# Optimization experiments

Hardware: AMD Instinct MI355X
Metric: run time of the kernel (lower is better)

## Reference

```python
import jax, jax.numpy as jnp
import numpy as np

FFT_SIZE = 16384

def setup_inputs() -> dict:
    key = jax.random.key(0)
    k1, k2 = jax.random.split(key)
    u = jax.random.normal(k1, (8, 1024, 8192), dtype=jnp.float32)
    k = jax.random.normal(k2, (1024, 8192), dtype=jnp.float32)
    return {"u": u, "k": k}

def reference(u, k):
    # Faithful port of PyTorchFFTConv.forward with fft_size=FFT_SIZE.
    L = u.shape[-1]
    u_f32 = u.astype(jnp.float32)
    k_f32 = k.astype(jnp.float32)
    if k_f32.ndim == 2:
        k_f32 = k_f32[None]  # (1, H, L) -> broadcasts over batch
    u_fft = jnp.fft.rfft(u_f32, n=FFT_SIZE, axis=-1)   # (B, H, fft/2+1) complex64
    k_fft = jnp.fft.rfft(k_f32, n=FFT_SIZE, axis=-1)
    y_fft = u_fft * k_fft / FFT_SIZE
    # irfft with norm='forward' (no 1/n on inverse) combined with the /fft_s above
    # yields the standard circular convolution, matching the torch code exactly.
    y = jnp.fft.irfft(y_fft, n=FFT_SIZE, axis=-1, norm='forward')
    return y[..., :L].astype(jnp.float32)
```

## Files before the change

### kernel.cpp

```cpp
#include <hip/hip_runtime.h>

#define NFFT 16384
#define LSIG 8192
#define NH   1024
#define NTH  512
#define LDSC (NFFT + ((NFFT >> 5) << 1))

__device__ __forceinline__ int PADC(int i) { return i + ((i >> 5) << 1); }
__device__ __forceinline__ int PADI(int i) { return i + (i >> 5); }

struct cplx { float x, y; };
__device__ __forceinline__ cplx cadd(cplx a, cplx b){ return {a.x+b.x, a.y+b.y}; }
__device__ __forceinline__ cplx csub(cplx a, cplx b){ return {a.x-b.x, a.y-b.y}; }
__device__ __forceinline__ cplx cmul(cplx a, cplx b){ return {a.x*b.x - a.y*b.y, a.x*b.y + a.y*b.x}; }

template<int V> struct ic { static constexpr int value = V; };
template<int Start, int End, typename F>
__device__ __forceinline__ void cfor(F&& f) {
  if constexpr (Start < End) { f(ic<Start>{}); cfor<Start+1, End>(static_cast<F&&>(f)); }
}

constexpr float W32C32[32] = {
  1.0f, 0.9807852804f, 0.9238795325f, 0.8314696123f,
  0.7071067812f, 0.5555702330f, 0.3826834324f, 0.1950903220f,
  0.0f, -0.1950903220f, -0.3826834324f, -0.5555702330f,
  -0.7071067812f, -0.8314696123f, -0.9238795325f, -0.9807852804f,
  -1.0f, -0.9807852804f, -0.9238795325f, -0.8314696123f,
  -0.7071067812f, -0.5555702330f, -0.3826834324f, -0.1950903220f,
  0.0f, 0.1950903220f, 0.3826834324f, 0.5555702330f,
  0.7071067812f, 0.8314696123f, 0.9238795325f, 0.9807852804f };
constexpr float W32S32[32] = {
  0.0f, 0.1950903220f, 0.3826834324f, 0.5555702330f,
  0.7071067812f, 0.8314696123f, 0.9238795325f, 0.9807852804f,
  1.0f, 0.9807852804f, 0.9238795325f, 0.8314696123f,
  0.7071067812f, 0.5555702330f, 0.3826834324f, 0.1950903220f,
  0.0f, -0.1950903220f, -0.3826834324f, -0.5555702330f,
  -0.7071067812f, -0.8314696123f, -0.9238795325f, -0.9807852804f,
  -1.0f, -0.9807852804f, -0.9238795325f, -0.8314696123f,
  -0.7071067812f, -0.5555702330f, -0.3826834324f, -0.1950903220f };
constexpr int BR3[8] = {0,4,2,6,1,5,3,7};

template<int KK, bool INV>
__device__ __forceinline__ cplx twid(cplx d) {
  constexpr int K = KK & 31;
  if constexpr (K == 0)       return d;
  else if constexpr (K == 8)  { if constexpr (INV) return cplx{-d.y, d.x}; else return cplx{d.y, -d.x}; }
  else if constexpr (K == 16) return cplx{-d.x, -d.y};
  else if constexpr (K == 24) { if constexpr (INV) return cplx{d.y, -d.x}; else return cplx{-d.y, d.x}; }
  else {
    constexpr float c = W32C32[K];
    constexpr float s = INV ? W32S32[K] : -W32S32[K];
    return cmul(d, cplx{c, s});
  }
}

template<int N, int SP, bool INV>
__device__ __forceinline__ void fft_pass(cplx* z) {
  #pragma unroll
  for (int b = 0; b < N; b += 2*SP) {
    cfor<0, SP>([&](auto rc){
      constexpr int r = decltype(rc)::value;
      constexpr int KK = r * (16 / SP);
      if constexpr (!INV) {
        cplx u = z[b+r], v = z[b+r+SP];
        z[b+r]    = cadd(u, v);
        z[b+r+SP] = twid<KK,false>(csub(u, v));
      } else {
        cplx t0 = z[b+r], t1 = z[b+r+SP];
        cplx w = twid<KK,true>(t1);
        z[b+r]    = cadd(t0, w);
        z[b+r+SP] = csub(t0, w);
      }
    });
  }
}

template<int N, bool INV>
__device__ __forceinline__ void fft_regs(cplx* z) {
  if constexpr (!INV) {
    if constexpr (N >= 32) fft_pass<N,16,false>(z);
    if constexpr (N >= 16) fft_pass<N, 8,false>(z);
    if constexpr (N >=  8) fft_pass<N, 4,false>(z);
    if constexpr (N >=  4) fft_pass<N, 2,false>(z);
    fft_pass<N,1,false>(z);
  } else {
    fft_pass<N,1,true>(z);
    if constexpr (N >=  4) fft_pass<N, 2,true>(z);
    if constexpr (N >=  8) fft_pass<N, 4,true>(z);
    if constexpr (N >= 16) fft_pass<N, 8,true>(z);
    if constexpr (N >= 32) fft_pass<N,16,true>(z);
  }
}

template<int S, bool INV>
__device__ __forceinline__ void stage8p(float2* sz, int tid) {
  const float ang1 = (INV ? 2.0f : -2.0f) * 3.14159265358979f / (float)(8 * S);
  #pragma unroll 1
  for (int it = 0; it < 2; ++it) {
    int pp = tid + it * NTH;
    int bf = 2 * pp;
    int q = bf / S;
    int r = bf - q * S;
    int base = q * (8 * S) + r;
    float ta = ang1 * (float)r;
    float tb = ang1 * (float)(r + 1);
    cplx w1a = {__cosf(ta), __sinf(ta)};
    cplx w1b = {__cosf(tb), __sinf(tb)};
    cplx wa[8], wb[8];
    wa[1]=w1a; wa[2]=cmul(w1a,w1a); wa[3]=cmul(wa[2],w1a); wa[4]=cmul(wa[2],wa[2]);
    wa[5]=cmul(wa[4],wa[1]); wa[6]=cmul(wa[4],wa[2]); wa[7]=cmul(wa[4],wa[3]);
    wb[1]=w1b; wb[2]=cmul(w1b,w1b); wb[3]=cmul(wb[2],w1b); wb[4]=cmul(wb[2],wb[2]);
    wb[5]=cmul(wb[4],wb[1]); wb[6]=cmul(wb[4],wb[2]); wb[7]=cmul(wb[4],wb[3]);

    cplx A[8], B[8];
    if constexpr (!INV) {
      cfor<0,8>([&](auto jc){ constexpr int j = decltype(jc)::value;
        float4 v = *reinterpret_cast<const float4*>(&sz[PADC(base + j*S)]);
        A[j] = {v.x, v.y}; B[j] = {v.z, v.w}; });
      fft_regs<8,false>(A);
      fft_regs<8,false>(B);
      cfor<0,8>([&](auto pc){ constexpr int p = decltype(pc)::value;
        constexpr int m = BR3[p];
        cplx oa, ob;
        if constexpr (m == 0) { oa = A[p]; ob = B[p]; }
        else { oa = cmul(A[p], wa[m]); ob = cmul(B[p], wb[m]); }
        *reinterpret_cast<float4*>(&sz[PADC(base + m*S)]) = make_float4(oa.x, oa.y, ob.x, ob.y); });
    } else {
      cfor<0,8>([&](auto pc){ constexpr int p = decltype(pc)::value;
        constexpr int m = BR3[p];
        float4 v = *reinterpret_cast<const float4*>(&sz[PADC(base + m*S)]);
        if constexpr (m == 0) { A[p] = {v.x, v.y}; B[p] = {v.z, v.w}; }
        else { A[p] = cmul(cplx{v.x, v.y}, wa[m]); B[p] = cmul(cplx{v.z, v.w}, wb[m]); } });
      fft_regs<8,true>(A);
      fft_regs<8,true>(B);
      cfor<0,8>([&](auto jc){ constexpr int j = decltype(jc)::value;
        *reinterpret_cast<float4*>(&sz[PADC(base + j*S)]) = make_float4(A[j].x, A[j].y, B[j].x, B[j].y); });
    }
  }
}

template<bool INV>
__device__ __forceinline__ void stage8_s4p(float2* sz, int tid) {
  cfor<0,2>([&](auto rrc){
    constexpr int r0 = decltype(rrc)::value * 2;
    int base = tid * 32 + r0;
    cplx A[8], B[8];
    if constexpr (!INV) {
      cfor<0,8>([&](auto jc){ constexpr int j = decltype(jc)::value;
        float4 v = *reinterpret_cast<const float4*>(&sz[PADC(base + j*4)]);
        A[j] = {v.x, v.y}; B[j] = {v.z, v.w}; });
      fft_regs<8,false>(A);
      fft_regs<8,false>(B);
      cfor<0,8>([&](auto pc){ constexpr int p = decltype(pc)::value;
        constexpr int m = BR3[p];
        cplx oa = twid<r0*m, false>(A[p]);
        cplx ob = twid<(r0+1)*m, false>(B[p]);
        *reinterpret_cast<float4*>(&sz[PADC(base + m*4)]) = make_float4(oa.x, oa.y, ob.x, ob.y); });
    } else {
      cfor<0,8>([&](auto pc){ constexpr int p = decltype(pc)::value;
        constexpr int m = BR3[p];
        float4 v = *reinterpret_cast<const float4*>(&sz[PADC(base + m*4)]);
        A[p] = twid<r0*m, true>(cplx{v.x, v.y});
        B[p] = twid<(r0+1)*m, true>(cplx{v.z, v.w}); });
      fft_regs<8,true>(A);
      fft_regs<8,true>(B);
      cfor<0,8>([&](auto jc){ constexpr int j = decltype(jc)::value;
        *reinterpret_cast<float4*>(&sz[PADC(base + j*4)]) = make_float4(A[j].x, A[j].y, B[j].x, B[j].y); });
    }
  });
}

__global__ __launch_bounds__(NTH)
void kfft_kernel(const float* __restrict__ kin, float2* __restrict__ kh) {
  __shared__ __align__(16) float2 sz[LDSC];
  const int tid = threadIdx.x;
  const int h = blockIdx.x;
  const float* krow = kin + (size_t)h * LSIG;
  #pragma unroll
  for (int c = 0; c < 8; ++c) {
    int ci = (c * NTH + tid) * 2;
    float2 v = *reinterpret_cast<const float2*>(krow + ci);
    *reinterpret_cast<float4*>(&sz[PADC(ci)]) = make_float4(v.x, 0.f, v.y, 0.f);
    *reinterpret_cast<float4*>(&sz[PADC(ci + LSIG)]) = make_float4(0.f, 0.f, 0.f, 0.f);
  }
  __syncthreads();
  stage8p<2048,false>(sz, tid); __syncthreads();
  stage8p< 256,false>(sz, tid); __syncthreads();
  stage8p<  32,false>(sz, tid); __syncthreads();
  stage8_s4p<false>(sz, tid);   __syncthreads();

  const float scl = 1.0f / (float)NFFT;
  float2* row = kh + (size_t)h * NFFT;
  #pragma unroll
  for (int s = 0; s < 8; ++s) {
    int m = tid + NTH * s;
    int ci = 4 * m;
    float4 f0 = *reinterpret_cast<const float4*>(&sz[PADC(ci)]);
    float4 f1 = *reinterpret_cast<const float4*>(&sz[PADC(ci + 2)]);
    cplx z[4] = { {f0.x, f0.y}, {f0.z, f0.w}, {f1.x, f1.y}, {f1.z, f1.w} };
    fft_regs<4,false>(z);
    *reinterpret_cast<float4*>(row + ci)     = make_float4(z[0].x*scl, z[0].y*scl, z[1].x*scl, z[1].y*scl);
    *reinterpret_cast<float4*>(row + ci + 2) = make_float4(z[2].x*scl, z[2].y*scl, z[3].x*scl, z[3].y*scl);
  }
}

__global__ __launch_bounds__(NTH)
void conv_kernel(const float* __restrict__ u, const float2* __restrict__ kh,
                 float* __restrict__ out) {
  __shared__ __align__(16) float2 sz[LDSC];
  const int tid = threadIdx.x;
  const int bid = blockIdx.x;
  const int h  = bid >> 2;
  const int pr = bid & 3;

  const float* u0 = u + ((size_t)(2*pr) * NH + h) * LSIG;
  const float* u1 = u0 + (size_t)NH * LSIG;
  #pragma unroll
  for (int c = 0; c < 8; ++c) {
    int ci = (c * NTH + tid) * 2;
    float2 a = *reinterpret_cast<const float2*>(u0 + ci);
    float2 b = *reinterpret_cast<const float2*>(u1 + ci);
    *reinterpret_cast<float4*>(&sz[PADC(ci)]) = make_float4(a.x, b.x, a.y, b.y);
    *reinterpret_cast<float4*>(&sz[PADC(ci + LSIG)]) = make_float4(0.f, 0.f, 0.f, 0.f);
  }
  __syncthreads();
  stage8p<2048,false>(sz, tid); __syncthreads();
  stage8p< 256,false>(sz, tid); __syncthreads();
  stage8p<  32,false>(sz, tid); __syncthreads();
  stage8_s4p<false>(sz, tid);   __syncthreads();

  {
    const float2* krow = kh + (size_t)h * NFFT;
    #pragma unroll
    for (int s = 0; s < 8; ++s) {
      int m = tid + NTH * s;
      int ci = 4 * m;
      float4 f0 = *reinterpret_cast<const float4*>(&sz[PADC(ci)]);
      float4 f1 = *reinterpret_cast<const float4*>(&sz[PADC(ci + 2)]);
      cplx z[4] = { {f0.x, f0.y}, {f0.z, f0.w}, {f1.x, f1.y}, {f1.z, f1.w} };
      fft_regs<4,false>(z);
      float4 k0 = *reinterpret_cast<const float4*>(krow + ci);
      float4 k1 = *reinterpret_cast<const float4*>(krow + ci + 2);
      z[0] = cmul(z[0], cplx{k0.x, k0.y});
      z[1] = cmul(z[1], cplx{k0.z, k0.w});
      z[2] = cmul(z[2], cplx{k1.x, k1.y});
      z[3] = cmul(z[3], cplx{k1.z, k1.w});
      fft_regs<4,true>(z);
      *reinterpret_cast<float4*>(&sz[PADC(ci)])     = make_float4(z[0].x, z[0].y, z[1].x, z[1].y);
      *reinterpret_cast<float4*>(&sz[PADC(ci + 2)]) = make_float4(z[2].x, z[2].y, z[3].x, z[3].y);
    }
  }
  __syncthreads();
  stage8_s4p<true>(sz, tid);   __syncthreads();
  stage8p<  32,true>(sz, tid); __syncthreads();
  stage8p< 256,true>(sz, tid); __syncthreads();
  stage8p<2048,true>(sz, tid); __syncthreads();

  float* o0 = out + ((size_t)(2*pr) * NH + h) * LSIG;
  float* o1 = o0 + (size_t)NH * LSIG;
  #pragma unroll
  for (int c = 0; c < 4; ++c) {
    int ci = (c * NTH + tid) * 4;
    float4 f0 = *reinterpret_cast<const float4*>(&sz[PADC(ci)]);
    float4 f1 = *reinterpret_cast<const float4*>(&sz[PADC(ci + 2)]);
    *reinterpret_cast<float4*>(o0 + ci) = make_float4(f0.x, f0.z, f1.x, f1.z);
    *reinterpret_cast<float4*>(o1 + ci) = make_float4(f0.y, f0.w, f1.y, f1.w);
  }
}

template<int S, bool INV>
__device__ __forceinline__ void stage8f(float* sre, float* sim, int tid) {
  const float ang1 = (INV ? 2.0f : -2.0f) * 3.14159265358979f / (float)(8 * S);
  #pragma unroll
  for (int it = 0; it < (NFFT/8)/NTH; ++it) {
    int bf = tid + it * NTH;
    int q = bf / S;
    int r = bf - q * S;
    int base = q * (8 * S) + r;
    float t = ang1 * (float)r;
    cplx w1 = {__cosf(t), __sinf(t)};
    cplx wp[8];
    wp[0] = {1.0f, 0.0f};
    wp[1] = w1; wp[2] = cmul(w1, w1); wp[3] = cmul(wp[2], w1); wp[4] = cmul(wp[2], wp[2]);
    wp[5] = cmul(wp[4], wp[1]); wp[6] = cmul(wp[4], wp[2]); wp[7] = cmul(wp[4], wp[3]);
    cplx a[8];
    if constexpr (!INV) {
      cfor<0,8>([&](auto jc){ constexpr int j = decltype(jc)::value;
        int idx = PADI(base + j*S); a[j] = {sre[idx], sim[idx]}; });
      fft_regs<8,false>(a);
      cfor<0,8>([&](auto pc){ constexpr int p = decltype(pc)::value;
        constexpr int m = BR3[p];
        cplx o; if constexpr (m == 0) o = a[p]; else o = cmul(a[p], wp[m]);
        int idx = PADI(base + m*S); sre[idx] = o.x; sim[idx] = o.y; });
    } else {
      cfor<0,8>([&](auto pc){ constexpr int p = decltype(pc)::value;
        constexpr int m = BR3[p];
        int idx = PADI(base + m*S); cplx v = {sre[idx], sim[idx]};
        if constexpr (m == 0) a[p] = v; else a[p] = cmul(v, wp[m]); });
      fft_regs<8,true>(a);
      cfor<0,8>([&](auto jc){ constexpr int j = decltype(jc)::value;
        int idx = PADI(base + j*S); sre[idx] = a[j].x; sim[idx] = a[j].y; });
    }
  }
}

template<bool INV>
__device__ __forceinline__ void stage8_s4f(float* sre, float* sim, int tid) {
  cfor<0,4>([&](auto rc){
    constexpr int r = decltype(rc)::value;
    int base = tid * 32 + r;
    cplx a[8];
    if constexpr (!INV) {
      cfor<0,8>([&](auto jc){ constexpr int j = decltype(jc)::value;
        int idx = PADI(base + j*4); a[j] = {sre[idx], sim[idx]}; });
      fft_regs<8,false>(a);
      cfor<0,8>([&](auto pc){ constexpr int p = decltype(pc)::value;
        constexpr int m = BR3[p];
        cplx o = twid<r*m, false>(a[p]);
        int idx = PADI(base + m*4); sre[idx] = o.x; sim[idx] = o.y; });
    } else {
      cfor<0,8>([&](auto pc){ constexpr int p = decltype(pc)::value;
        constexpr int m = BR3[p];
        int idx = PADI(base + m*4); cplx v = {sre[idx], sim[idx]};
        a[p] = twid<r*m, true>(v); });
      fft_regs<8,true>(a);
      cfor<0,8>([&](auto jc){ constexpr int j = decltype(jc)::value;
        int idx = PADI(base + j*4); sre[idx] = a[j].x; sim[idx] = a[j].y; });
    }
  });
}

__global__ __launch_bounds__(NTH)
void fftconv_fallback(const float* __restrict__ u, const float* __restrict__ kin,
                      float* __restrict__ out) {
  __shared__ float sre[NFFT + (NFFT >> 5)];
  __shared__ float sim[NFFT + (NFFT >> 5)];
  const int tid = threadIdx.x;
  const int bid = blockIdx.x;
  const int h  = bid >> 2;
  const int pr = bid & 3;

  const float* krow = kin + (size_t)h * LSIG;
  #pragma unroll
  for (int c = 0; c < 4; ++c) {
    int i0 = (c * NTH + tid) * 4;
    float4 v = *reinterpret_cast<const float4*>(krow + i0);
    int p0 = PADI(i0);
    sre[p0+0]=v.x; sre[p0+1]=v.y; sre[p0+2]=v.z; sre[p0+3]=v.w;
    sim[p0+0]=0.f; sim[p0+1]=0.f; sim[p0+2]=0.f; sim[p0+3]=0.f;
    int p1 = PADI(i0 + LSIG);
    sre[p1+0]=0.f; sre[p1+1]=0.f; sre[p1+2]=0.f; sre[p1+3]=0.f;
    sim[p1+0]=0.f; sim[p1+1]=0.f; sim[p1+2]=0.f; sim[p1+3]=0.f;
  }
  __syncthreads();
  stage8f<2048,false>(sre, sim, tid); __syncthreads();
  stage8f< 256,false>(sre, sim, tid); __syncthreads();
  stage8f<  32,false>(sre, sim, tid); __syncthreads();
  stage8_s4f<false>(sre, sim, tid);   __syncthreads();

  cplx kq[4][4];
  cplx kq2[4][4];
  const float scl = 1.0f / (float)NFFT;
  #pragma unroll
  for (int s = 0; s < 8; ++s) {
    int m = tid + NTH * s;
    int p = PADI(4 * m);
    cplx z[4] = { {sre[p+0], sim[p+0]}, {sre[p+1], sim[p+1]},
                  {sre[p+2], sim[p+2]}, {sre[p+3], sim[p+3]} };
    fft_regs<4,false>(z);
    #pragma unroll
    for (int e = 0; e < 4; ++e) {
      cplx v = {z[e].x*scl, z[e].y*scl};
      if (s < 4) kq[s][e] = v; else kq2[s-4][e] = v;
    }
  }
  __syncthreads();

  const float* u0 = u + ((size_t)(2*pr) * NH + h) * LSIG;
  const float* u1 = u0 + (size_t)NH * LSIG;
  #pragma unroll
  for (int c = 0; c < 4; ++c) {
    int i0 = (c * NTH + tid) * 4;
    float4 a = *reinterpret_cast<const float4*>(u0 + i0);
    float4 b = *reinterpret_cast<const float4*>(u1 + i0);
    int p0 = PADI(i0);
    sre[p0+0]=a.x; sre[p0+1]=a.y; sre[p0+2]=a.z; sre[p0+3]=a.w;
    sim[p0+0]=b.x; sim[p0+1]=b.y; sim[p0+2]=b.z; sim[p0+3]=b.w;
    int p1 = PADI(i0 + LSIG);
    sre[p1+0]=0.f; sre[p1+1]=0.f; sre[p1+2]=0.f; sre[p1+3]=0.f;
    sim[p1+0]=0.f; sim[p1+1]=0.f; sim[p1+2]=0.f; sim[p1+3]=0.f;
  }
  __syncthreads();
  stage8f<2048,false>(sre, sim, tid); __syncthreads();
  stage8f< 256,false>(sre, sim, tid); __syncthreads();
  stage8f<  32,false>(sre, sim, tid); __syncthreads();
  stage8_s4f<false>(sre, sim, tid);   __syncthreads();

  #pragma unroll
  for (int s = 0; s < 8; ++s) {
    int m = tid + NTH * s;
    int p = PADI(4 * m);
    cplx z[4] = { {sre[p+0], sim[p+0]}, {sre[p+1], sim[p+1]},
                  {sre[p+2], sim[p+2]}, {sre[p+3], sim[p+3]} };
    fft_regs<4,false>(z);
    #pragma unroll
    for (int e = 0; e < 4; ++e) z[e] = cmul(z[e], (s<4) ? kq[s][e] : kq2[s-4][e]);
    fft_regs<4,true>(z);
    #pragma unroll
    for (int e = 0; e < 4; ++e) { sre[p+e] = z[e].x; sim[p+e] = z[e].y; }
  }
  __syncthreads();
  stage8_s4f<true>(sre, sim, tid);   __syncthreads();
  stage8f<  32,true>(sre, sim, tid); __syncthreads();
  stage8f< 256,true>(sre, sim, tid); __syncthreads();
  stage8f<2048,true>(sre, sim, tid); __syncthreads();

  float* o0 = out + ((size_t)(2*pr) * NH + h) * LSIG;
  float* o1 = o0 + (size_t)NH * LSIG;
  #pragma unroll
  for (int c = 0; c < 4; ++c) {
    int i0 = (c * NTH + tid) * 4;
    int p0 = PADI(i0);
    float4 a = {sre[p0], sre[p0+1], sre[p0+2], sre[p0+3]};
    float4 b = {sim[p0], sim[p0+1], sim[p0+2], sim[p0+3]};
    *reinterpret_cast<float4*>(o0 + i0) = a;
    *reinterpret_cast<float4*>(o1 + i0) = b;
  }
}

extern "C" void kernel_launch(void* const* d_in, const int* in_sizes, int n_in,
                              void* d_out, int out_size, void* d_ws, size_t ws_size,
                              hipStream_t stream) {
  (void)in_sizes; (void)n_in; (void)out_size;
  const float* u = (const float*)d_in[0];
  const float* k = (const float*)d_in[1];
  float* out = (float*)d_out;
  const size_t need = (size_t)NH * NFFT * sizeof(float2);
  if (ws_size >= need) {
    hipLaunchKernelGGL(kfft_kernel, dim3(NH),   dim3(NTH), 0, stream, k, (float2*)d_ws);
    hipLaunchKernelGGL(conv_kernel, dim3(4096), dim3(NTH), 0, stream, u, (const float2*)d_ws, out);
  } else {
    hipLaunchKernelGGL(fftconv_fallback, dim3(4096), dim3(NTH), 0, stream, u, k, out);
  }
}
```

Baseline: 444.6 us.

## Fuse first FFT stage with global load and last inverse stage with store

The first radix-8 stage is now computed in registers straight from global memory. It exploits the zero-padded upper half, so only 4 inputs per butterfly are loaded and the LDS zero-fill is skipped. The final inverse stage is fused with the output write and computes only the needed first half of outputs. The last-stage data mapping is also changed so each thread owns contiguous chunks, which drops two barriers around the pointwise multiply. The cost is extra register pressure and a less coalesced global access pattern (strided float2 loads per thread).

```diff
diff --git a/kernel.cpp b/kernel.cpp
--- a/kernel.cpp
+++ b/kernel.cpp
@@ -176,25 +176,45 @@
   const int tid = threadIdx.x;
   const int h = blockIdx.x;
   const float* krow = kin + (size_t)h * LSIG;
-  #pragma unroll
-  for (int c = 0; c < 8; ++c) {
-    int ci = (c * NTH + tid) * 2;
-    float2 v = *reinterpret_cast<const float2*>(krow + ci);
-    *reinterpret_cast<float4*>(&sz[PADC(ci)]) = make_float4(v.x, 0.f, v.y, 0.f);
-    *reinterpret_cast<float4*>(&sz[PADC(ci + LSIG)]) = make_float4(0.f, 0.f, 0.f, 0.f);
-  }
-  __syncthreads();
-  stage8p<2048,false>(sz, tid); __syncthreads();
+  const float ang1 = -2.0f * 3.14159265358979f / (float)NFFT;
+
+  #pragma unroll 1
+  for (int it = 0; it < 2; ++it) {
+    int base = 2*tid + 1024*it;
+    cplx A[8], B[8];
+    cfor<0,4>([&](auto jc){ constexpr int j = decltype(jc)::value;
+      float2 kr = *reinterpret_cast<const float2*>(krow + base + j*2048);
+      A[j] = {kr.x, 0.f}; B[j] = {kr.y, 0.f}; });
+    cfor<0,4>([&](auto jc){ constexpr int j = decltype(jc)::value;
+      A[j+4] = twid<4*j,false>(A[j]);
+      B[j+4] = twid<4*j,false>(B[j]); });
+    fft_pass<8,2,false>(A); fft_pass<8,1,false>(A);
+    fft_pass<8,2,false>(B); fft_pass<8,1,false>(B);
+    float ta = ang1 * (float)base, tb = ang1 * (float)(base + 1);
+    cplx w1a = {__cosf(ta), __sinf(ta)};
+    cplx w1b = {__cosf(tb), __sinf(tb)};
+    cplx wa[8], wb[8];
+    wa[1]=w1a; wa[2]=cmul(w1a,w1a); wa[3]=cmul(wa[2],w1a); wa[4]=cmul(wa[2],wa[2]);
+    wa[5]=cmul(wa[4],wa[1]); wa[6]=cmul(wa[4],wa[2]); wa[7]=cmul(wa[4],wa[3]);
+    wb[1]=w1b; wb[2]=cmul(w1b,w1b); wb[3]=cmul(wb[2],w1b); wb[4]=cmul(wb[2],wb[2]);
+    wb[5]=cmul(wb[4],wb[1]); wb[6]=cmul(wb[4],wb[2]); wb[7]=cmul(wb[4],wb[3]);
+    cfor<0,8>([&](auto pc){ constexpr int p = decltype(pc)::value;
+      constexpr int m = BR3[p];
+      cplx oa, ob;
+      if constexpr (m == 0) { oa = A[p]; ob = B[p]; }
+      else { oa = cmul(A[p], wa[m]); ob = cmul(B[p], wb[m]); }
+      *reinterpret_cast<float4*>(&sz[PADC(base + m*2048)]) = make_float4(oa.x, oa.y, ob.x, ob.y); });
+  }
+  __syncthreads();
   stage8p< 256,false>(sz, tid); __syncthreads();
   stage8p<  32,false>(sz, tid); __syncthreads();
-  stage8_s4p<false>(sz, tid);   __syncthreads();
+  stage8_s4p<false>(sz, tid);
 
   const float scl = 1.0f / (float)NFFT;
   float2* row = kh + (size_t)h * NFFT;
   #pragma unroll
   for (int s = 0; s < 8; ++s) {
-    int m = tid + NTH * s;
-    int ci = 4 * m;
+    int ci = 32*tid + 4*s;
     float4 f0 = *reinterpret_cast<const float4*>(&sz[PADC(ci)]);
     float4 f1 = *reinterpret_cast<const float4*>(&sz[PADC(ci + 2)]);
     cplx z[4] = { {f0.x, f0.y}, {f0.z, f0.w}, {f1.x, f1.y}, {f1.z, f1.w} };
@@ -215,26 +235,50 @@
 
   const float* u0 = u + ((size_t)(2*pr) * NH + h) * LSIG;
   const float* u1 = u0 + (size_t)NH * LSIG;
-  #pragma unroll
-  for (int c = 0; c < 8; ++c) {
-    int ci = (c * NTH + tid) * 2;
-    float2 a = *reinterpret_cast<const float2*>(u0 + ci);
-    float2 b = *reinterpret_cast<const float2*>(u1 + ci);
-    *reinterpret_cast<float4*>(&sz[PADC(ci)]) = make_float4(a.x, b.x, a.y, b.y);
-    *reinterpret_cast<float4*>(&sz[PADC(ci + LSIG)]) = make_float4(0.f, 0.f, 0.f, 0.f);
-  }
-  __syncthreads();
-  stage8p<2048,false>(sz, tid); __syncthreads();
+  float* o0 = out + ((size_t)(2*pr) * NH + h) * LSIG;
+  float* o1 = o0 + (size_t)NH * LSIG;
+
+  {
+    const float ang1 = -2.0f * 3.14159265358979f / (float)NFFT;
+    #pragma unroll 1
+    for (int it = 0; it < 2; ++it) {
+      int base = 2*tid + 1024*it;
+      cplx A[8], B[8];
+      cfor<0,4>([&](auto jc){ constexpr int j = decltype(jc)::value;
+        float2 a2 = *reinterpret_cast<const float2*>(u0 + base + j*2048);
+        float2 b2 = *reinterpret_cast<const float2*>(u1 + base + j*2048);
+        A[j] = {a2.x, b2.x}; B[j] = {a2.y, b2.y}; });
+      cfor<0,4>([&](auto jc){ constexpr int j = decltype(jc)::value;
+        A[j+4] = twid<4*j,false>(A[j]);
+        B[j+4] = twid<4*j,false>(B[j]); });
+      fft_pass<8,2,false>(A); fft_pass<8,1,false>(A);
+      fft_pass<8,2,false>(B); fft_pass<8,1,false>(B);
+      float ta = ang1 * (float)base, tb = ang1 * (float)(base + 1);
+      cplx w1a = {__cosf(ta), __sinf(ta)};
+      cplx w1b = {__cosf(tb), __sinf(tb)};
+      cplx wa[8], wb[8];
+      wa[1]=w1a; wa[2]=cmul(w1a,w1a); wa[3]=cmul(wa[2],w1a); wa[4]=cmul(wa[2],wa[2]);
+      wa[5]=cmul(wa[4],wa[1]); wa[6]=cmul(wa[4],wa[2]); wa[7]=cmul(wa[4],wa[3]);
+      wb[1]=w1b; wb[2]=cmul(w1b,w1b); wb[3]=cmul(wb[2],w1b); wb[4]=cmul(wb[2],wb[2]);
+      wb[5]=cmul(wb[4],wb[1]); wb[6]=cmul(wb[4],wb[2]); wb[7]=cmul(wb[4],wb[3]);
+      cfor<0,8>([&](auto pc){ constexpr int p = decltype(pc)::value;
+        constexpr int m = BR3[p];
+        cplx oa, ob;
+        if constexpr (m == 0) { oa = A[p]; ob = B[p]; }
+        else { oa = cmul(A[p], wa[m]); ob = cmul(B[p], wb[m]); }
+        *reinterpret_cast<float4*>(&sz[PADC(base + m*2048)]) = make_float4(oa.x, oa.y, ob.x, ob.y); });
+    }
+  }
+  __syncthreads();
   stage8p< 256,false>(sz, tid); __syncthreads();
   stage8p<  32,false>(sz, tid); __syncthreads();
-  stage8_s4p<false>(sz, tid);   __syncthreads();
-
+
+  stage8_s4p<false>(sz, tid);
   {
     const float2* krow = kh + (size_t)h * NFFT;
     #pragma unroll
     for (int s = 0; s < 8; ++s) {
-      int m = tid + NTH * s;
-      int ci = 4 * m;
+      int ci = 32*tid + 4*s;
       float4 f0 = *reinterpret_cast<const float4*>(&sz[PADC(ci)]);
       float4 f1 = *reinterpret_cast<const float4*>(&sz[PADC(ci + 2)]);
       cplx z[4] = { {f0.x, f0.y}, {f0.z, f0.w}, {f1.x, f1.y}, {f1.z, f1.w} };
@@ -250,21 +294,38 @@
       *reinterpret_cast<float4*>(&sz[PADC(ci + 2)]) = make_float4(z[2].x, z[2].y, z[3].x, z[3].y);
     }
   }
-  __syncthreads();
-  stage8_s4p<true>(sz, tid);   __syncthreads();
+  stage8_s4p<true>(sz, tid);
+  __syncthreads();
   stage8p<  32,true>(sz, tid); __syncthreads();
   stage8p< 256,true>(sz, tid); __syncthreads();
-  stage8p<2048,true>(sz, tid); __syncthreads();
-
-  float* o0 = out + ((size_t)(2*pr) * NH + h) * LSIG;
-  float* o1 = o0 + (size_t)NH * LSIG;
-  #pragma unroll
-  for (int c = 0; c < 4; ++c) {
-    int ci = (c * NTH + tid) * 4;
-    float4 f0 = *reinterpret_cast<const float4*>(&sz[PADC(ci)]);
-    float4 f1 = *reinterpret_cast<const float4*>(&sz[PADC(ci + 2)]);
-    *reinterpret_cast<float4*>(o0 + ci) = make_float4(f0.x, f0.z, f1.x, f1.z);
-    *reinterpret_cast<float4*>(o1 + ci) = make_float4(f0.y, f0.w, f1.y, f1.w);
+
+  {
+    const float ang1 = 2.0f * 3.14159265358979f / (float)NFFT;
+    #pragma unroll 1
+    for (int it = 0; it < 2; ++it) {
+      int base = 2*tid + 1024*it;
+      float ta = ang1 * (float)base, tb = ang1 * (float)(base + 1);
+      cplx w1a = {__cosf(ta), __sinf(ta)};
+      cplx w1b = {__cosf(tb), __sinf(tb)};
+      cplx wa[8], wb[8];
+      wa[1]=w1a; wa[2]=cmul(w1a,w1a); wa[3]=cmul(wa[2],w1a); wa[4]=cmul(wa[2],wa[2]);
+      wa[5]=cmul(wa[4],wa[1]); wa[6]=cmul(wa[4],wa[2]); wa[7]=cmul(wa[4],wa[3]);
+      wb[1]=w1b; wb[2]=cmul(w1b,w1b); wb[3]=cmul(wb[2],w1b); wb[4]=cmul(wb[2],wb[2]);
+      wb[5]=cmul(wb[4],wb[1]); wb[6]=cmul(wb[4],wb[2]); wb[7]=cmul(wb[4],wb[3]);
+      cplx A[8], B[8];
+      cfor<0,8>([&](auto pc){ constexpr int p = decltype(pc)::value;
+        constexpr int m = BR3[p];
+        float4 v = *reinterpret_cast<const float4*>(&sz[PADC(base + m*2048)]);
+        if constexpr (m == 0) { A[p] = {v.x, v.y}; B[p] = {v.z, v.w}; }
+        else { A[p] = cmul(cplx{v.x, v.y}, wa[m]); B[p] = cmul(cplx{v.z, v.w}, wb[m]); } });
+      fft_pass<8,1,true>(A); fft_pass<8,2,true>(A);
+      fft_pass<8,1,true>(B); fft_pass<8,2,true>(B);
+      cfor<0,4>([&](auto rc){ constexpr int r = decltype(rc)::value;
+        cplx yA = cadd(A[r], twid<4*r,true>(A[r+4]));
+        cplx yB = cadd(B[r], twid<4*r,true>(B[r+4]));
+        *reinterpret_cast<float2*>(o0 + base + r*2048) = make_float2(yA.x, yB.x);
+        *reinterpret_cast<float2*>(o1 + base + r*2048) = make_float2(yA.y, yB.y); });
+    }
   }
 }
 
```

Result: faster. 431.0 us (-3.1%).
